# Performance work log

Hardware: AMD Instinct MI355X
Metric: run time of the kernel (lower is better)

## Reference

```python
import jax, jax.numpy as jnp
import numpy as np

B, S, J, L, E, H, NI, NT = 8, 32, 4, 32, 500, 500, 5000, 48


def _lstm_scan(x, h0, c0, Wi, Wh, b):
    # x: [T, ..., E]; torch LSTM gate order i,f,g,o
    def step(carry, xt):
        h, c = carry
        z = xt @ Wi.T + h @ Wh.T + b
        i, f, g, o = jnp.split(z, 4, axis=-1)
        c = jax.nn.sigmoid(f) * c + jax.nn.sigmoid(i) * jnp.tanh(g)
        h = jax.nn.sigmoid(o) * jnp.tanh(c)
        return (h, c), h
    (h, c), hs = jax.lax.scan(step, (h0, c0), x)
    return hs, (h, c)


def setup_inputs() -> dict:
    key = jax.random.key(0)
    ks = jax.random.split(key, 24)
    p = lambda k, shp: jax.random.normal(k, shp, jnp.float32) * 0.05
    t = jnp.arange(S)
    return dict(
        item_vectors=jax.random.randint(ks[0], (B, S), 0, NI),
        sequence_tim=jax.random.randint(ks[1], (B, S), 0, NT),
        dilated_idx=jax.random.randint(ks[2], (B, S), 0, S) % jnp.maximum(t, 1)[None, :],
        hist_items=jax.random.randint(ks[3], (B, J, L), 0, NI),
        hist_tims=jax.random.randint(ks[4], (B, J, L), 0, NT),
        mask=jnp.ones((B, S), jnp.float32),
        tim_sim=jax.random.uniform(ks[5], (NT, NT)),
        poi_dist=jax.random.uniform(ks[6], (NI, NI)) + 0.1,
        emb_W=p(ks[7], (NI, E)),
        lstm_Wi=p(ks[8], (4 * H, E)), lstm_Wh=p(ks[9], (4 * H, H)), lstm_b=jnp.zeros((4 * H,)),
        hist_Wi=p(ks[10], (4 * H, E)), hist_Wh=p(ks[11], (4 * H, H)), hist_b=jnp.zeros((4 * H,)),
        dil_Wi=p(ks[12], (4 * H, E)), dil_Wh=p(ks[13], (4 * H, H)), dil_b=jnp.zeros((4 * H,)),
        lin1_W=p(ks[14], (H, H)), lin1_b=jnp.zeros((H,)),
        lin_W=p(ks[15], (NI, 2 * H)), lin_b=jnp.zeros((NI,)),
    )


def _fwd(item_vectors, sequence_tim, dilated_idx, hist_items, hist_tims, mask,
         tim_sim, poi_dist, emb_W, lstm_Wi, lstm_Wh, lstm_b, hist_Wi, hist_Wh,
         hist_b, dil_Wi, dil_Wh, dil_b, lin1_W, lin1_b, lin_W, lin_b):
    items = emb_W[item_vectors]                                  # [B,S,E]
    hs, _ = _lstm_scan(items.transpose(1, 0, 2), jnp.zeros((B, H)), jnp.zeros((B, H)),
                       lstm_Wi, lstm_Wh, lstm_b)
    out = hs.transpose(1, 0, 2)                                  # [B,S,H]

    def dilated_one(xb, idx):
        # dilated LSTMCell: prev state gathered from data-dependent index (zeros at t=0)
        def step(carry, inp):
            Hs, Cs = carry
            t, it, xt = inp
            ph = jnp.where(t == 0, jnp.zeros((H,)), Hs[it])
            pc = jnp.where(t == 0, jnp.zeros((H,)), Cs[it])
            z = xt @ dil_Wi.T + ph @ dil_Wh.T + dil_b
            i, f, g, o = jnp.split(z, 4)
            c = jax.nn.sigmoid(f) * pc + jax.nn.sigmoid(i) * jnp.tanh(g)
            h = jax.nn.sigmoid(o) * jnp.tanh(c)
            return (Hs.at[t].set(h), Cs.at[t].set(c)), None
        (Hs, _), _ = jax.lax.scan(step, (jnp.zeros((S, H)), jnp.zeros((S, H))),
                                  (jnp.arange(S), idx, xb))
        return Hs
    out_hie = jax.vmap(dilated_one)(items, dilated_idx)          # [B,S,H]

    # train-branch session representation: masked mean, same at every step
    denom = jnp.sum(mask, axis=1, keepdims=True)
    pooled = jnp.sum(out * mask[:, :, None], axis=1) / denom     # [B,H]
    csr = jnp.broadcast_to(pooled[:, None, :], (B, S - 1, H))

    def hist_one(items_j, tims_j, timid, poiid, csr_b, out_b):
        jac_rows = tim_sim[timid]                                # [S-1,NT]
        dist_rows = poi_dist[poiid]                              # [S-1,NI]
        def sess_step(carry, inp):
            h2, c2 = carry
            itms, tms = inp
            he, (h2, c2) = _lstm_scan(emb_W[itms], h2, c2, hist_Wi, hist_Wh, hist_b)
            w = jax.nn.softmax(jac_rows[:, tms], axis=1)         # [S-1,L]
            sess_rep = w @ he                                    # [S-1,H]
            avg_d = jnp.mean(dist_rows[:, itms], axis=1)         # [S-1]
            return (h2, c2), (sess_rep, avg_d)
        _, (sess, avgd) = jax.lax.scan(sess_step, (jnp.zeros((H,)), jnp.zeros((H,))),
                                       (items_j, tims_j))
        sess_t = sess.transpose(1, 0, 2)                         # [S-1,J,H]
        avgd_t = avgd.T                                          # [S-1,J]
        sims = jax.nn.softmax(jnp.einsum('sjh,sh->sj', sess_t, csr_b), axis=1)
        out_y = jax.nn.selu(jnp.einsum('sj,sjh->sh', sims, sess_t) @ lin1_W.T + lin1_b)
        layer2 = 0.5 * out_y + 0.5 * out_b[:S - 1]
        l2s = jax.nn.softmax(jnp.einsum('sjh,sh->sj', sess_t, layer2) / avgd_t, axis=1)
        ol2 = jnp.einsum('sj,sjh->sh', l2s, sess_t)              # [S-1,H]
        return jnp.concatenate([ol2, jnp.zeros((1, H))], axis=0)  # pad to [S,H]

    y = jax.nn.selu(jax.vmap(hist_one)(hist_items, hist_tims, sequence_tim[:, :S - 1],
                                       item_vectors[:, :S - 1], csr, out))
    out_mix = 0.5 * (jax.nn.selu(out) + jax.nn.selu(out_hie))
    logits = jnp.concatenate([y, out_mix], axis=2) @ lin_W.T + lin_b
    return jax.nn.log_softmax(logits, axis=-1)


def reference(item_vectors, sequence_tim, dilated_idx, hist_items, hist_tims, mask,
              tim_sim, poi_dist, emb_W, lstm_Wi, lstm_Wh, lstm_b, hist_Wi, hist_Wh,
              hist_b, dil_Wi, dil_Wh, dil_b, lin1_W, lin1_b, lin_W, lin_b):
    return _fwd(item_vectors, sequence_tim, dilated_idx, hist_items, hist_tims, mask,
                tim_sim, poi_dist, emb_W, lstm_Wi, lstm_Wh, lstm_b, hist_Wi, hist_Wh,
                hist_b, dil_Wi, dil_Wh, dil_b, lin1_W, lin1_b, lin_W, lin_b)
```

## Files before the change

kernel.cpp:

```cpp
#include <hip/hip_runtime.h>
#include <hip/hip_bf16.h>
#include <math.h>

#define B_ 8
#define S_ 32
#define J_ 4
#define L_ 32
#define E_ 500
#define H_ 500
#define NI_ 5000
#define NT_ 48
#define G4_ 2000

#define NB_ 25
#define RPB_ 20
#define TPB_ 640

typedef unsigned long long ull;

__device__ __forceinline__ float sigm(float x) { return 1.f / (1.f + expf(-x)); }
__device__ __forceinline__ float seluf(float x) {
    const float sc = 1.0507009873554805f, al = 1.6732632423543772f;
    return x > 0.f ? sc * x : sc * al * (expf(x) - 1.f);
}
__device__ __forceinline__ float cohload(const float* p) {
    return __hip_atomic_load(p, __ATOMIC_RELAXED, __HIP_MEMORY_SCOPE_AGENT);
}
__device__ __forceinline__ ull cohload64(const ull* p) {
    return __hip_atomic_load(p, __ATOMIC_RELAXED, __HIP_MEMORY_SCOPE_AGENT);
}
__device__ __forceinline__ void cohstore(float* p, float v) {
    __hip_atomic_store(p, v, __ATOMIC_RELAXED, __HIP_MEMORY_SCOPE_AGENT);
}

__global__ void k_zero(int* p, int n) {
    int i = blockIdx.x * blockDim.x + threadIdx.x;
    if (i < n) __hip_atomic_store(&p[i], 0, __ATOMIC_RELAXED, __HIP_MEMORY_SCOPE_AGENT);
}

__global__ __launch_bounds__(128) void k_embed(const int* __restrict__ itemv,
                                               const int* __restrict__ histi,
                                               const float* __restrict__ embW,
                                               float* __restrict__ items,
                                               float* __restrict__ histemb) {
    int row = blockIdx.x;
    int id;
    float* dst;
    if (row < 256) { id = itemv[row]; dst = items + (size_t)row * E_; }
    else           { int rr = row - 256; id = histi[rr]; dst = histemb + (size_t)rr * E_; }
    const float4* s = (const float4*)(embW + (size_t)id * E_);
    float4* d = (float4*)dst;
    if (threadIdx.x < 125) d[threadIdx.x] = s[threadIdx.x];
}

#define TBM 64
#define TBN 64
#define TBK 16
__global__ __launch_bounds__(256) void k_gemm_bt(const float* __restrict__ A,
                                                 const float* __restrict__ Bm,
                                                 const float* __restrict__ bias,
                                                 float* __restrict__ C,
                                                 int M, int N, int K) {
    __shared__ float As[TBK][TBM + 1];
    __shared__ float Bs[TBK][TBN + 1];
    const int tid = threadIdx.x;
    const int tx = tid & 15, ty = tid >> 4;
    const int row0 = blockIdx.y * TBM, col0 = blockIdx.x * TBN;
    float acc[4][4] = {};
    for (int k0 = 0; k0 < K; k0 += TBK) {
#pragma unroll
        for (int i = 0; i < 4; ++i) {
            int e = tid + i * 256;
            int kk = e & 15, m = e >> 4;
            int gk = k0 + kk;
            float va = 0.f, vb = 0.f;
            int gm = row0 + m, gn = col0 + m;
            if (gk < K) {
                if (gm < M) va = A[(size_t)gm * K + gk];
                if (gn < N) vb = Bm[(size_t)gn * K + gk];
            }
            As[kk][m] = va;
            Bs[kk][m] = vb;
        }
        __syncthreads();
#pragma unroll
        for (int kk = 0; kk < TBK; ++kk) {
            float a[4], bb[4];
#pragma unroll
            for (int i = 0; i < 4; ++i) a[i] = As[kk][ty * 4 + i];
#pragma unroll
            for (int i = 0; i < 4; ++i) bb[i] = Bs[kk][tx * 4 + i];
#pragma unroll
            for (int i = 0; i < 4; ++i)
#pragma unroll
                for (int j = 0; j < 4; ++j) acc[i][j] += a[i] * bb[j];
        }
        __syncthreads();
    }
#pragma unroll
    for (int i = 0; i < 4; ++i) {
        int gm = row0 + ty * 4 + i;
        if (gm >= M) continue;
#pragma unroll
        for (int j = 0; j < 4; ++j) {
            int gn = col0 + tx * 4 + j;
            if (gn < N) C[(size_t)gm * N + gn] = acc[i][j] + (bias ? bias[gn] : 0.f);
        }
    }
}

__global__ __launch_bounds__(TPB_) void k_rec6(
    const float* __restrict__ xwm, const float* __restrict__ Whm,
    const float* __restrict__ xwd, const float* __restrict__ Whd,
    const int* __restrict__ dilidx,
    const float* __restrict__ xwh, const float* __restrict__ Whh,
    float* __restrict__ outm, float* __restrict__ outh,
    float* __restrict__ csg, float* __restrict__ he,
    int* __restrict__ flags) {
    __shared__ __align__(16) float h_s[8][500];
    __shared__ __align__(16) float4 part4[4][RPB_][8];
    __shared__ float c_s[RPB_][8];
    float* hflat = &h_s[0][0];
    const int tid = threadIdx.x;
    const int gb = blockIdx.x;
    const int role = gb / NB_;
    const int blk = gb - role * NB_;
    const int r0 = blk * RPB_;

    const float* Wh   = (role == 0) ? Whm : (role == 1) ? Whd : Whh;
    const float* xw   = (role == 0) ? xwm : (role == 1) ? xwd : xwh;
    const float* exch = (role == 0) ? outm : (role == 1) ? outh : he;
    const int nsteps  = (role == 2) ? 128 : 32;
    const int rstride = (role == 2) ? 128 : S_;
    int* flag = flags + role * 32;

    const int ksec = tid / 160;
    const int rr   = tid - ksec * 160;
    const int q    = rr >> 3;
    const int b    = rr & 7;
    const int hi   = r0 + q;
    const int kbase = ksec * 128;
    const int n4    = (ksec < 3) ? 32 : 29;

    const float4* wp0 = (const float4*)(Wh + (size_t)(0 * 500 + hi) * 500 + kbase);
    const float4* wp1 = (const float4*)(Wh + (size_t)(1 * 500 + hi) * 500 + kbase);
    const float4* wp2 = (const float4*)(Wh + (size_t)(2 * 500 + hi) * 500 + kbase);
    const float4* wp3 = (const float4*)(Wh + (size_t)(3 * 500 + hi) * 500 + kbase);

    const int e0 = tid;
    const int bb0 = e0 / 125, k40 = e0 - bb0 * 125;

    if (tid < 160) c_s[q][b] = 0.f;

    for (int t = 0; t < nsteps; ++t) {
        float xwv0 = 0.f, xwv1 = 0.f, xwv2 = 0.f, xwv3 = 0.f;
        if (tid < 160) {
            const float* xr = xw + (size_t)(b * nsteps + t) * G4_ + hi;
            xwv0 = xr[0]; xwv1 = xr[500]; xwv2 = xr[1000]; xwv3 = xr[1500];
        }

        float pc_r = 0.f;
        if (t > 0) {
            if (tid < 64) {
                while (true) {
                    int v = (tid < NB_)
                        ? __hip_atomic_load(&flag[tid], __ATOMIC_RELAXED,
                                            __HIP_MEMORY_SCOPE_AGENT)
                        : 0x7fffffff;
                    if (__all(v >= t)) break;
                    __builtin_amdgcn_s_sleep(1);
                }
            }
            __syncthreads();

            if (role == 1 && tid < 160) {
                int it = dilidx[b * S_ + t];
                pc_r = cohload(&csg[((size_t)(b * S_ + it)) * H_ + hi]);
            }

            if (tid < 500) {
                int row0 = (role == 1) ? dilidx[bb0 * S_ + t] : (t - 1);
                int row1 = (role == 1) ? dilidx[(bb0 + 4) * S_ + t] : (t - 1);
                const ull* p0 = (const ull*)(exch + ((size_t)(bb0 * rstride + row0)) * H_ + k40 * 4);
                const ull* p1 = (const ull*)(exch + ((size_t)((bb0 + 4) * rstride + row1)) * H_ + k40 * 4);
                ull a0 = cohload64(p0);
                ull a1 = cohload64(p0 + 1);
                ull a2 = cohload64(p1);
                ull a3 = cohload64(p1 + 1);
                union { ull u[2]; float4 f; } u0, u1;
                u0.u[0] = a0; u0.u[1] = a1;
                u1.u[0] = a2; u1.u[1] = a3;
                *(float4*)&hflat[(size_t)e0 * 4]         = u0.f;
                *(float4*)&hflat[(size_t)(e0 + 500) * 4] = u1.f;
            }
            __syncthreads();

            const float4* hp = (const float4*)(&h_s[b][kbase]);
            float a0 = 0.f, a1 = 0.f, a2 = 0.f, a3 = 0.f;
#pragma unroll 2
            for (int k4 = 0; k4 < n4; ++k4) {
                float4 hv = hp[k4];
                float4 w0 = wp0[k4], w1 = wp1[k4], w2 = wp2[k4], w3 = wp3[k4];
                a0 += w0.x * hv.x + w0.y * hv.y + w0.z * hv.z + w0.w * hv.w;
                a1 += w1.x * hv.x + w1.y * hv.y + w1.z * hv.z + w1.w * hv.w;
                a2 += w2.x * hv.x + w2.y * hv.y + w2.z * hv.z + w2.w * hv.w;
                a3 += w3.x * hv.x + w3.y * hv.y + w3.z * hv.z + w3.w * hv.w;
            }
            part4[ksec][q][b] = make_float4(a0, a1, a2, a3);
        }
        __syncthreads();

        if (tid < 160) {
            float zi = xwv0, zf = xwv1, zg = xwv2, zo = xwv3;
            if (t > 0) {
                float4 p0 = part4[0][q][b], p1 = part4[1][q][b];
                float4 p2 = part4[2][q][b], p3 = part4[3][q][b];
                zi += (p0.x + p1.x) + (p2.x + p3.x);
                zf += (p0.y + p1.y) + (p2.y + p3.y);
                zg += (p0.z + p1.z) + (p2.z + p3.z);
                zo += (p0.w + p1.w) + (p2.w + p3.w);
            }
            float pc = (role == 1) ? pc_r : c_s[q][b];
            float cc = sigm(zf) * pc + sigm(zi) * tanhf(zg);
            float hh = sigm(zo) * tanhf(cc);
            if (role == 0) {
                c_s[q][b] = cc;
                cohstore(&outm[((size_t)(b * S_ + t)) * H_ + hi], hh);
            } else if (role == 2) {
                c_s[q][b] = cc;
                cohstore(&he[((size_t)(b * 128 + t)) * H_ + hi], hh);
            } else {
                cohstore(&outh[((size_t)(b * S_ + t)) * H_ + hi], hh);
                cohstore(&csg[((size_t)(b * S_ + t)) * H_ + hi], cc);
            }
        }
        __syncthreads();
        if (tid == 0)
            __hip_atomic_store(&flag[blk], t + 1, __ATOMIC_RELAXED,
                               __HIP_MEMORY_SCOPE_AGENT);
    }
}

__global__ __launch_bounds__(512) void k_pool(const float* __restrict__ outm,
                                              const float* __restrict__ mask,
                                              float* __restrict__ pooled) {
    int b = blockIdx.x, tid = threadIdx.x;
    if (tid >= 500) return;
    float acc = 0.f, den = 0.f;
    for (int s = 0; s < S_; ++s) {
        float mk = mask[b * S_ + s];
        acc += outm[((size_t)(b * S_ + s)) * H_ + tid] * mk;
        den += mk;
    }
    pooled[b * H_ + tid] = acc / den;
}

__global__ __launch_bounds__(512) void k_sess(const int* __restrict__ seqtim,
                                              const int* __restrict__ itemv,
                                              const int* __restrict__ histt,
                                              const int* __restrict__ histi,
                                              const float* __restrict__ timsim,
                                              const float* __restrict__ poid,
                                              const float* __restrict__ he,
                                              float* __restrict__ sess,
                                              float* __restrict__ avgd) {
    int bi = blockIdx.x;
    int s = bi % 31;
    int tmpv = bi / 31;
    int j = tmpv & 3, b = tmpv >> 2;
    __shared__ float w[L_];
    __shared__ float pd[L_];
    __shared__ float stats[1];
    int tid = threadIdx.x;
    int st = seqtim[b * S_ + s];
    if (tid < L_) {
        int ht = histt[(b * J_ + j) * L_ + tid];
        w[tid] = timsim[st * NT_ + ht];
    }
    if (tid >= 64 && tid < 64 + L_) {
        int l = tid - 64;
        int iv = itemv[b * S_ + s];
        pd[l] = poid[(size_t)iv * NI_ + histi[(b * J_ + j) * L_ + l]];
    }
    __syncthreads();
    if (tid == 64) {
        float a = 0.f;
        for (int l = 0; l < L_; ++l) a += pd[l];
        avgd[(b * J_ + j) * 31 + s] = a * (1.f / 32.f);
    }
    if (tid == 0) {
        float m = -1e30f;
        for (int l = 0; l < L_; ++l) m = fmaxf(m, w[l]);
        float sm = 0.f;
        for (int l = 0; l < L_; ++l) { float e = expf(w[l] - m); w[l] = e; sm += e; }
        stats[0] = 1.f / sm;
    }
    __syncthreads();
    if (tid < 500) {
        float inv = stats[0];
        float acc = 0.f;
        const float* hp = he + ((size_t)(b * J_ * L_ + j * L_)) * H_ + tid;
        for (int l = 0; l < L_; ++l) acc += w[l] * inv * hp[(size_t)l * H_];
        sess[((size_t)((b * J_ + j) * 31 + s)) * H_ + tid] = acc;
    }
}

__global__ __launch_bounds__(512) void k_att1(const float* __restrict__ sess,
                                              const float* __restrict__ pooled,
                                              float* __restrict__ att1) {
    int bi = blockIdx.x;
    int s = bi % 31, b = bi / 31;
    __shared__ float vec[H_];
    __shared__ float part[512];
    int tid = threadIdx.x;
    if (tid < 500) vec[tid] = pooled[b * H_ + tid];
    __syncthreads();
    int j = tid >> 7, i = tid & 127;
    const float* sp = sess + ((size_t)((b * J_ + j) * 31 + s)) * H_;
    float acc = 0.f;
    for (int h = i; h < H_; h += 128) acc += sp[h] * vec[h];
    part[tid] = acc;
    __syncthreads();
    for (int off = 64; off > 0; off >>= 1) {
        if (i < off) part[tid] += part[tid + off];
        __syncthreads();
    }
    float d0 = part[0], d1 = part[128], d2 = part[256], d3 = part[384];
    float m = fmaxf(fmaxf(d0, d1), fmaxf(d2, d3));
    float e0 = expf(d0 - m), e1 = expf(d1 - m), e2 = expf(d2 - m), e3 = expf(d3 - m);
    float inv = 1.f / (e0 + e1 + e2 + e3);
    if (tid < 500) {
        const float* s0 = sess + ((size_t)(b * J_ * 31 + s)) * H_ + tid;
        const size_t js = (size_t)31 * H_;
        float r = e0 * inv * s0[0] + e1 * inv * s0[js] + e2 * inv * s0[2 * js] + e3 * inv * s0[3 * js];
        att1[((size_t)(b * 31 + s)) * H_ + tid] = r;
    }
}

__global__ __launch_bounds__(512) void k_att2(const float* __restrict__ sess,
                                              const float* __restrict__ outy,
                                              const float* __restrict__ outm,
                                              const float* __restrict__ avgd,
                                              float* __restrict__ X) {
    int bi = blockIdx.x;
    int s = bi % 31, b = bi / 31;
    __shared__ float vec[H_];
    __shared__ float part[512];
    int tid = threadIdx.x;
    if (tid < 500)
        vec[tid] = 0.5f * seluf(outy[((size_t)(b * 31 + s)) * H_ + tid]) +
                   0.5f * outm[((size_t)(b * S_ + s)) * H_ + tid];
    __syncthreads();
    int j = tid >> 7, i = tid & 127;
    const float* sp = sess + ((size_t)((b * J_ + j) * 31 + s)) * H_;
    float acc = 0.f;
    for (int h = i; h < H_; h += 128) acc += sp[h] * vec[h];
    part[tid] = acc;
    __syncthreads();
    for (int off = 64; off > 0; off >>= 1) {
        if (i < off) part[tid] += part[tid + off];
        __syncthreads();
    }
    float d0 = part[0]   / avgd[(b * J_ + 0) * 31 + s];
    float d1 = part[128] / avgd[(b * J_ + 1) * 31 + s];
    float d2 = part[256] / avgd[(b * J_ + 2) * 31 + s];
    float d3 = part[384] / avgd[(b * J_ + 3) * 31 + s];
    float m = fmaxf(fmaxf(d0, d1), fmaxf(d2, d3));
    float e0 = expf(d0 - m), e1 = expf(d1 - m), e2 = expf(d2 - m), e3 = expf(d3 - m);
    float inv = 1.f / (e0 + e1 + e2 + e3);
    if (tid < 500) {
        const float* s0 = sess + ((size_t)(b * J_ * 31 + s)) * H_ + tid;
        const size_t js = (size_t)31 * H_;
        float r = e0 * inv * s0[0] + e1 * inv * s0[js] + e2 * inv * s0[2 * js] + e3 * inv * s0[3 * js];
        X[((size_t)(b * S_ + s)) * 1000 + tid] = seluf(r);
    }
}

__global__ __launch_bounds__(512) void k_mix(const float* __restrict__ outm,
                                             const float* __restrict__ outh,
                                             float* __restrict__ X) {
    int bs = blockIdx.x;
    int tid = threadIdx.x;
    if (tid >= 500) return;
    size_t idx = (size_t)bs * H_ + tid;
    float om = 0.5f * (seluf(outm[idx]) + seluf(outh[idx]));
    X[(size_t)bs * 1000 + 500 + tid] = om;
    if ((bs & (S_ - 1)) == S_ - 1) X[(size_t)bs * 1000 + tid] = 0.f;
}

__global__ __launch_bounds__(512) void k_lsm(float* __restrict__ out) {
    int row = blockIdx.x, tid = threadIdx.x;
    float* p = out + (size_t)row * NI_;
    __shared__ float red[512];
    float m = -1e30f;
    for (int i = tid; i < NI_; i += 512) m = fmaxf(m, p[i]);
    red[tid] = m;
    __syncthreads();
    for (int off = 256; off > 0; off >>= 1) {
        if (tid < off) red[tid] = fmaxf(red[tid], red[tid + off]);
        __syncthreads();
    }
    m = red[0];
    __syncthreads();
    float sm = 0.f;
    for (int i = tid; i < NI_; i += 512) sm += expf(p[i] - m);
    red[tid] = sm;
    __syncthreads();
    for (int off = 256; off > 0; off >>= 1) {
        if (tid < off) red[tid] += red[tid + off];
        __syncthreads();
    }
    float lse = m + logf(red[0]);
    __syncthreads();
    for (int i = tid; i < NI_; i += 512) p[i] -= lse;
}

extern "C" void kernel_launch(void* const* d_in, const int* in_sizes, int n_in,
                              void* d_out, int out_size, void* d_ws, size_t ws_size,
                              hipStream_t stream) {
    const int* item_vectors = (const int*)d_in[0];
    const int* sequence_tim = (const int*)d_in[1];
    const int* dilated_idx  = (const int*)d_in[2];
    const int* hist_items   = (const int*)d_in[3];
    const int* hist_tims    = (const int*)d_in[4];
    const float* mask       = (const float*)d_in[5];
    const float* tim_sim    = (const float*)d_in[6];
    const float* poi_dist   = (const float*)d_in[7];
    const float* emb_W      = (const float*)d_in[8];
    const float* lstm_Wi    = (const float*)d_in[9];
    const float* lstm_Wh    = (const float*)d_in[10];
    const float* lstm_b     = (const float*)d_in[11];
    const float* hist_Wi    = (const float*)d_in[12];
    const float* hist_Wh    = (const float*)d_in[13];
    const float* hist_b     = (const float*)d_in[14];
    const float* dil_Wi     = (const float*)d_in[15];
    const float* dil_Wh     = (const float*)d_in[16];
    const float* dil_b      = (const float*)d_in[17];
    const float* lin1_W     = (const float*)d_in[18];
    const float* lin1_b     = (const float*)d_in[19];
    const float* lin_W      = (const float*)d_in[20];
    const float* lin_b      = (const float*)d_in[21];
    float* out = (float*)d_out;
    float* ws  = (float*)d_ws;

    float* items   = ws + 0;
    float* histemb = ws + 128000;
    float* xwm     = ws + 640000;
    float* xwd     = ws + 1152000;
    float* xwh     = ws + 1664000;
    float* outm    = ws + 3712000;
    float* outh    = ws + 3840000;
    float* csg     = ws + 3968000;
    float* he      = ws + 4096000;
    float* pooled  = ws + 4608000;
    float* sess    = ws + 4612000;
    float* avgd    = ws + 5108000;
    float* att1    = ws + 5108992;
    float* outy    = ws + 5232992;
    float* Xbuf    = ws + 5356992;
    int*   flags   = (int*)(ws + 5612992);

    k_zero<<<dim3(1), dim3(128), 0, stream>>>(flags, 96);
    k_embed<<<dim3(1280), dim3(128), 0, stream>>>(item_vectors, hist_items, emb_W, items, histemb);

    k_gemm_bt<<<dim3(32, 4), dim3(256), 0, stream>>>(items, lstm_Wi, lstm_b, xwm, 256, G4_, E_);
    k_gemm_bt<<<dim3(32, 4), dim3(256), 0, stream>>>(items, dil_Wi, dil_b, xwd, 256, G4_, E_);
    k_gemm_bt<<<dim3(32, 16), dim3(256), 0, stream>>>(histemb, hist_Wi, hist_b, xwh, 1024, G4_, E_);

    k_rec6<<<dim3(3 * NB_), dim3(TPB_), 0, stream>>>(
        xwm, lstm_Wh, xwd, dil_Wh, dilated_idx, xwh, hist_Wh,
        outm, outh, csg, he, flags);

    k_pool<<<dim3(B_), dim3(512), 0, stream>>>(outm, mask, pooled);
    k_sess<<<dim3(B_ * J_ * 31), dim3(512), 0, stream>>>(sequence_tim, item_vectors, hist_tims,
                                                         hist_items, tim_sim, poi_dist, he, sess, avgd);
    k_att1<<<dim3(B_ * 31), dim3(512), 0, stream>>>(sess, pooled, att1);
    k_gemm_bt<<<dim3(8, 4), dim3(256), 0, stream>>>(att1, lin1_W, lin1_b, outy, 248, H_, H_);
    k_att2<<<dim3(B_ * 31), dim3(512), 0, stream>>>(sess, outy, outm, avgd, Xbuf);
    k_mix<<<dim3(B_ * S_), dim3(512), 0, stream>>>(outm, outh, Xbuf);

    k_gemm_bt<<<dim3(79, 4), dim3(256), 0, stream>>>(Xbuf, lin_W, lin_b, out, 256, NI_, 1000);
    k_lsm<<<dim3(256), dim3(512), 0, stream>>>(out);
}
```

Before: 2.072 ms.

## Restructure recurrent kernel to fewer larger blocks with shuffle reduction and padded flags

The recurrent LSTM kernel now runs 16 blocks of 1024 threads per role instead of 25 blocks of 640. Each thread's k-slice partial sums are reduced with warp shuffles rather than through shared memory. The cell state lives in registers, which removes one block barrier per timestep. Each block's progress flag is padded onto its own cache line to cut contention during the inter-block spin-wait. The trade-offs are that the last block handles clamped padded rows, the gate math is computed redundantly across the four k-sections, and fewer blocks now share the weight-streaming work.

```diff
diff --git a/kernel.cpp b/kernel.cpp
--- a/kernel.cpp
+++ b/kernel.cpp
@@ -12,9 +12,10 @@
 #define NT_ 48
 #define G4_ 2000
 
-#define NB_ 25
-#define RPB_ 20
-#define TPB_ 640
+#define NB_ 16
+#define RPB_ 32
+#define TPB_ 1024
+#define FPAD_ 32
 
 typedef unsigned long long ull;
 
@@ -109,7 +110,7 @@
     }
 }
 
-__global__ __launch_bounds__(TPB_) void k_rec6(
+__global__ __launch_bounds__(TPB_) void k_rec7(
     const float* __restrict__ xwm, const float* __restrict__ Whm,
     const float* __restrict__ xwd, const float* __restrict__ Whd,
     const int* __restrict__ dilidx,
@@ -118,13 +119,11 @@
     float* __restrict__ csg, float* __restrict__ he,
     int* __restrict__ flags) {
     __shared__ __align__(16) float h_s[8][500];
-    __shared__ __align__(16) float4 part4[4][RPB_][8];
-    __shared__ float c_s[RPB_][8];
     float* hflat = &h_s[0][0];
     const int tid = threadIdx.x;
     const int gb = blockIdx.x;
-    const int role = gb / NB_;
-    const int blk = gb - role * NB_;
+    const int role = gb >> 4;
+    const int blk = gb & (NB_ - 1);
     const int r0 = blk * RPB_;
 
     const float* Wh   = (role == 0) ? Whm : (role == 1) ? Whd : Whh;
@@ -132,71 +131,62 @@
     const float* exch = (role == 0) ? outm : (role == 1) ? outh : he;
     const int nsteps  = (role == 2) ? 128 : 32;
     const int rstride = (role == 2) ? 128 : S_;
-    int* flag = flags + role * 32;
-
-    const int ksec = tid / 160;
-    const int rr   = tid - ksec * 160;
-    const int q    = rr >> 3;
-    const int b    = rr & 7;
+    int* flag = flags + role * NB_ * FPAD_;
+
+    const int b    = tid & 7;
+    const int ksec = (tid >> 3) & 3;
+    const int q    = tid >> 5;
     const int hi   = r0 + q;
+    const int hic  = (hi < 500) ? hi : 499;
     const int kbase = ksec * 128;
     const int n4    = (ksec < 3) ? 32 : 29;
 
-    const float4* wp0 = (const float4*)(Wh + (size_t)(0 * 500 + hi) * 500 + kbase);
-    const float4* wp1 = (const float4*)(Wh + (size_t)(1 * 500 + hi) * 500 + kbase);
-    const float4* wp2 = (const float4*)(Wh + (size_t)(2 * 500 + hi) * 500 + kbase);
-    const float4* wp3 = (const float4*)(Wh + (size_t)(3 * 500 + hi) * 500 + kbase);
-
-    const int e0 = tid;
+    const float4* wp0 = (const float4*)(Wh + (size_t)(0 * 500 + hic) * 500 + kbase);
+    const float4* wp1 = (const float4*)(Wh + (size_t)(1 * 500 + hic) * 500 + kbase);
+    const float4* wp2 = (const float4*)(Wh + (size_t)(2 * 500 + hic) * 500 + kbase);
+    const float4* wp3 = (const float4*)(Wh + (size_t)(3 * 500 + hic) * 500 + kbase);
+
+    const int e0  = tid;
     const int bb0 = e0 / 125, k40 = e0 - bb0 * 125;
 
-    if (tid < 160) c_s[q][b] = 0.f;
+    float c_reg = 0.f;
 
     for (int t = 0; t < nsteps; ++t) {
-        float xwv0 = 0.f, xwv1 = 0.f, xwv2 = 0.f, xwv3 = 0.f;
-        if (tid < 160) {
-            const float* xr = xw + (size_t)(b * nsteps + t) * G4_ + hi;
-            xwv0 = xr[0]; xwv1 = xr[500]; xwv2 = xr[1000]; xwv3 = xr[1500];
-        }
-
+        const float* xr = xw + (size_t)(b * nsteps + t) * G4_ + hic;
+        float xi = xr[0], xf = xr[500], xg = xr[1000], xo = xr[1500];
+
+        float a0 = 0.f, a1 = 0.f, a2 = 0.f, a3 = 0.f;
         float pc_r = 0.f;
         if (t > 0) {
             if (tid < 64) {
                 while (true) {
                     int v = (tid < NB_)
-                        ? __hip_atomic_load(&flag[tid], __ATOMIC_RELAXED,
+                        ? __hip_atomic_load(&flag[tid * FPAD_], __ATOMIC_RELAXED,
                                             __HIP_MEMORY_SCOPE_AGENT)
                         : 0x7fffffff;
                     if (__all(v >= t)) break;
-                    __builtin_amdgcn_s_sleep(1);
+                    __builtin_amdgcn_s_sleep(2);
                 }
             }
             __syncthreads();
 
-            if (role == 1 && tid < 160) {
+            if (role == 1) {
                 int it = dilidx[b * S_ + t];
-                pc_r = cohload(&csg[((size_t)(b * S_ + it)) * H_ + hi]);
-            }
-
-            if (tid < 500) {
+                pc_r = cohload(&csg[((size_t)(b * S_ + it)) * H_ + hic]);
+            }
+
+            if (tid < 1000) {
                 int row0 = (role == 1) ? dilidx[bb0 * S_ + t] : (t - 1);
-                int row1 = (role == 1) ? dilidx[(bb0 + 4) * S_ + t] : (t - 1);
                 const ull* p0 = (const ull*)(exch + ((size_t)(bb0 * rstride + row0)) * H_ + k40 * 4);
-                const ull* p1 = (const ull*)(exch + ((size_t)((bb0 + 4) * rstride + row1)) * H_ + k40 * 4);
-                ull a0 = cohload64(p0);
-                ull a1 = cohload64(p0 + 1);
-                ull a2 = cohload64(p1);
-                ull a3 = cohload64(p1 + 1);
-                union { ull u[2]; float4 f; } u0, u1;
-                u0.u[0] = a0; u0.u[1] = a1;
-                u1.u[0] = a2; u1.u[1] = a3;
-                *(float4*)&hflat[(size_t)e0 * 4]         = u0.f;
-                *(float4*)&hflat[(size_t)(e0 + 500) * 4] = u1.f;
+                ull u0 = cohload64(p0);
+                ull u1 = cohload64(p0 + 1);
+                union { ull u[2]; float4 f; } uf;
+                uf.u[0] = u0; uf.u[1] = u1;
+                *(float4*)&hflat[(size_t)e0 * 4] = uf.f;
             }
             __syncthreads();
 
             const float4* hp = (const float4*)(&h_s[b][kbase]);
-            float a0 = 0.f, a1 = 0.f, a2 = 0.f, a3 = 0.f;
 #pragma unroll 2
             for (int k4 = 0; k4 < n4; ++k4) {
                 float4 hv = hp[k4];
@@ -206,37 +196,32 @@
                 a2 += w2.x * hv.x + w2.y * hv.y + w2.z * hv.z + w2.w * hv.w;
                 a3 += w3.x * hv.x + w3.y * hv.y + w3.z * hv.z + w3.w * hv.w;
             }
-            part4[ksec][q][b] = make_float4(a0, a1, a2, a3);
         }
-        __syncthreads();
-
-        if (tid < 160) {
-            float zi = xwv0, zf = xwv1, zg = xwv2, zo = xwv3;
-            if (t > 0) {
-                float4 p0 = part4[0][q][b], p1 = part4[1][q][b];
-                float4 p2 = part4[2][q][b], p3 = part4[3][q][b];
-                zi += (p0.x + p1.x) + (p2.x + p3.x);
-                zf += (p0.y + p1.y) + (p2.y + p3.y);
-                zg += (p0.z + p1.z) + (p2.z + p3.z);
-                zo += (p0.w + p1.w) + (p2.w + p3.w);
-            }
-            float pc = (role == 1) ? pc_r : c_s[q][b];
-            float cc = sigm(zf) * pc + sigm(zi) * tanhf(zg);
-            float hh = sigm(zo) * tanhf(cc);
+
+        a0 += __shfl_xor(a0, 8);  a0 += __shfl_xor(a0, 16);
+        a1 += __shfl_xor(a1, 8);  a1 += __shfl_xor(a1, 16);
+        a2 += __shfl_xor(a2, 8);  a2 += __shfl_xor(a2, 16);
+        a3 += __shfl_xor(a3, 8);  a3 += __shfl_xor(a3, 16);
+
+        float zi = xi + a0, zf = xf + a1, zg = xg + a2, zo = xo + a3;
+        float pc = (role == 1) ? pc_r : c_reg;
+        float cc = sigm(zf) * pc + sigm(zi) * tanhf(zg);
+        float hh = sigm(zo) * tanhf(cc);
+        c_reg = cc;
+
+        if (hi < 500) {
             if (role == 0) {
-                c_s[q][b] = cc;
-                cohstore(&outm[((size_t)(b * S_ + t)) * H_ + hi], hh);
+                if (ksec == 0) cohstore(&outm[((size_t)(b * S_ + t)) * H_ + hi], hh);
             } else if (role == 2) {
-                c_s[q][b] = cc;
-                cohstore(&he[((size_t)(b * 128 + t)) * H_ + hi], hh);
+                if (ksec == 0) cohstore(&he[((size_t)(b * 128 + t)) * H_ + hi], hh);
             } else {
-                cohstore(&outh[((size_t)(b * S_ + t)) * H_ + hi], hh);
-                cohstore(&csg[((size_t)(b * S_ + t)) * H_ + hi], cc);
+                if (ksec == 0) cohstore(&outh[((size_t)(b * S_ + t)) * H_ + hi], hh);
+                if (ksec == 1) cohstore(&csg[((size_t)(b * S_ + t)) * H_ + hi], cc);
             }
         }
         __syncthreads();
         if (tid == 0)
-            __hip_atomic_store(&flag[blk], t + 1, __ATOMIC_RELAXED,
+            __hip_atomic_store(&flag[blk * FPAD_], t + 1, __ATOMIC_RELAXED,
                                __HIP_MEMORY_SCOPE_AGENT);
     }
 }
@@ -460,14 +445,14 @@
     float* Xbuf    = ws + 5356992;
     int*   flags   = (int*)(ws + 5612992);
 
-    k_zero<<<dim3(1), dim3(128), 0, stream>>>(flags, 96);
+    k_zero<<<dim3(6), dim3(256), 0, stream>>>(flags, 3 * NB_ * FPAD_);
     k_embed<<<dim3(1280), dim3(128), 0, stream>>>(item_vectors, hist_items, emb_W, items, histemb);
 
     k_gemm_bt<<<dim3(32, 4), dim3(256), 0, stream>>>(items, lstm_Wi, lstm_b, xwm, 256, G4_, E_);
     k_gemm_bt<<<dim3(32, 4), dim3(256), 0, stream>>>(items, dil_Wi, dil_b, xwd, 256, G4_, E_);
     k_gemm_bt<<<dim3(32, 16), dim3(256), 0, stream>>>(histemb, hist_Wi, hist_b, xwh, 1024, G4_, E_);
 
-    k_rec6<<<dim3(3 * NB_), dim3(TPB_), 0, stream>>>(
+    k_rec7<<<dim3(3 * NB_), dim3(TPB_), 0, stream>>>(
         xwm, lstm_Wh, xwd, dil_Wh, dilated_idx, xwh, hist_Wh,
         outm, outh, csg, he, flags);
 
```

Measured after the change: 2.753 ms. 1.33x slower.
